# Optimization experiments

Hardware: AMD Instinct MI355X
Metric: run time of the kernel (lower is better)

Reference implementation:

```python
import jax, jax.numpy as jnp
import numpy as np

EPS = 2.220446049250313e-16  # sys.float_info.epsilon, matches CoCosNet feature_normalize

def feature_normalize(x):
    return x / (jnp.linalg.norm(x, axis=1, keepdims=True) + EPS)

def conv1x1(x, w, b):  # w: (out, in)
    return jnp.einsum('bchw,oc->bohw', x, w) + b[None, :, None, None]

def conv3x3(x, w, b):  # w: (out, in, 3, 3), SAME padding, stride 1
    y = jax.lax.conv_general_dilated(x, w, (1, 1), 'SAME',
                                     dimension_numbers=('NCHW', 'OIHW', 'NCHW'))
    return y + b[None, :, None, None]

@jax.custom_vjp
def sign_sig(x):
    return (x > 0).astype(x.dtype)

def _ss_fwd(x):
    return (x > 0).astype(x.dtype), jax.nn.sigmoid(x)

def _ss_bwd(s, g):
    return (g * s * (1.0 - s),)

sign_sig.defvjp(_ss_fwd, _ss_bwd)

def pono(x, eps=1e-5):  # PositionalNorm2d: normalize over channel dim
    m = jnp.mean(x, axis=1, keepdims=True)
    v = jnp.var(x, axis=1, keepdims=True)
    return (x - m) * jax.lax.rsqrt(v + eps)

def instance_norm(x, eps=1e-5):  # param-free, over spatial dims
    m = jnp.mean(x, axis=(2, 3), keepdims=True)
    v = jnp.var(x, axis=(2, 3), keepdims=True)
    return (x - m) * jax.lax.rsqrt(v + eps)

def setup_inputs() -> dict:
    B, CV, CPOS, H, W = 2, 256, 64, 64, 64
    CQK, DP, IC, NH = CV + CPOS, 64, 3, 128
    key = jax.random.key(0)
    ks = jax.random.split(key, 24)
    n = lambda i, s: jax.random.normal(ks[i], s, jnp.float32)
    w = lambda i, s: n(i, s) * 0.02
    z = lambda s: jnp.zeros(s, jnp.float32)
    return dict(
        q=n(0, (B, CV, H, W)), k=n(1, (B, CV, H, W)), v=n(2, (B, CV, H, W)),
        pos=n(3, (1, CPOS, H, W)),
        seg_map=jax.random.uniform(ks[4], (B, IC, H, W), jnp.float32),
        v2=n(5, (B, CV, H, W)),
        f_w=w(6, (CQK, CQK)), f_b=z(CQK),
        g_w=w(7, (CQK, CQK)), g_b=z(CQK),
        h_w=w(8, (CV, CV)), h_b=z(CV),
        fp_w=w(9, (DP, CQK)), fp_b=z(DP),
        gp_w=w(10, (DP, CQK)), gp_b=z(DP),
        sp_s_w=w(11, (NH, IC, 3, 3)), sp_s_b=z(NH),
        sp_g_w=w(12, (CV, NH, 3, 3)), sp_g_b=z(CV),
        sp_b_w=w(13, (CV, NH, 3, 3)), sp_b_b=z(CV),
        r1_w=w(14, (CV, CV, 3, 3)), r1_b=z(CV),
        r2_w=w(15, (CV, CV, 3, 3)), r2_b=z(CV),
    )

def reference(q, k, v, pos, seg_map, v2,
              f_w, f_b, g_w, g_b, h_w, h_b, fp_w, fp_b, gp_w, gp_b,
              sp_s_w, sp_s_b, sp_g_w, sp_g_b, sp_b_w, sp_b_b,
              r1_w, r1_b, r2_w, r2_b):
    b, cv, h, w = q.shape
    posb = jnp.broadcast_to(pos, (b,) + pos.shape[1:])
    query = jnp.concatenate([feature_normalize(q), posb], axis=1)
    keyt = jnp.concatenate([feature_normalize(k), posb], axis=1)
    qf = conv1x1(query, f_w, f_b)
    kf = conv1x1(keyt, g_w, g_b)
    vh = conv1x1(v, h_w, h_b)
    qp = conv1x1(query, fp_w, fp_b)
    kp = conv1x1(keyt, gp_w, gp_b)
    cqk = qf.shape[1]
    n = h * w
    Q = qf.reshape(b, cqk, n).transpose(0, 2, 1)          # (b, N, c_qk)
    K = kf.reshape(b, cqk, n)                             # (b, c_qk, N)
    V = vh.reshape(b, cv, n).transpose(0, 2, 1)           # (b, N, c_v)
    Qp = qp.reshape(b, -1, n).transpose(0, 2, 1)
    Kp = kp.reshape(b, -1, n)
    mask = sign_sig(jnp.einsum('bnc,bcm->bnm', Qp, Kp) / Kp.shape[1])
    cor = jnp.einsum('bnc,bcm->bnm', Q, K) / jnp.sqrt(jnp.float32(cqk))
    attn = jax.nn.softmax(cor, axis=-1)
    masked = attn * mask
    out = jnp.einsum('bnm,bmc->bnc', masked, V).transpose(0, 2, 1).reshape(b, cv, h, w)
    conf = masked.sum(-1).reshape(b, 1, h, w)
    V2 = v2.reshape(b, -1, n).transpose(0, 2, 1)
    attn2 = jax.nn.softmax(jnp.where(mask > 0, jnp.float32(-10000.0), cor), axis=-1)
    out2 = jnp.einsum('bnm,bmc->bnc', attn2, V2).transpose(0, 2, 1).reshape(b, -1, h, w)
    # SPADE(q, seg_map)
    actv = jax.nn.relu(conv3x3(seg_map, sp_s_w, sp_s_b))
    spade = instance_norm(q) * (1.0 + conv3x3(actv, sp_g_w, sp_g_b)) + conv3x3(actv, sp_b_w, sp_b_b)
    y = pono(out + (1.0 - conf) * spade + q)
    res = y + conv3x3(jax.nn.relu(conv3x3(y, r1_w, r1_b)), r2_w, r2_b)
    return (res, out2, cor)
```

## Files before the change

kernel.cpp:

```cpp
#include <hip/hip_runtime.h>
#include <stdint.h>


#define DEV static __device__ __forceinline__

typedef short short8 __attribute__((ext_vector_type(8)));
typedef float floatx4 __attribute__((ext_vector_type(4)));

DEV float bf2f(unsigned short b) { return __uint_as_float(((unsigned int)b) << 16); }
DEV unsigned short f2bf(float f) {
  unsigned int u = __float_as_uint(f);
  u += 0x7FFFu + ((u >> 16) & 1u);
  return (unsigned short)(u >> 16);
}
DEV float bfround(float f) { return bf2f(f2bf(f)); }

__global__ __launch_bounds__(256)
void cvt_f2b(const float* __restrict__ in, unsigned short* __restrict__ out, int n)
{
  int i = blockIdx.x * 256 + threadIdx.x;
  if (i < n) out[i] = f2bf(in[i]);
}

__global__ __launch_bounds__(256)
void prep_w9(const float* __restrict__ w, unsigned short* __restrict__ w9,
             int CO, int CI)
{
  int i = blockIdx.x * 256 + threadIdx.x;
  int tot = CO * CI * 9;
  if (i >= tot) return;
  int s = i % 9, rest = i / 9;
  int ci = rest % CI, o = rest / CI;
  w9[(long long)o * 9 * CI + s * CI + ci] = f2bf(w[i]);
}

__global__ __launch_bounds__(256)
void build_qk(const float* __restrict__ x, const float* __restrict__ pos,
              unsigned short* __restrict__ qt)
{
  int n = blockIdx.x, b = blockIdx.y, t = threadIdx.x;
  float v = x[((long long)(b * 256 + t) << 12) + n];
  __shared__ float red[256];
  red[t] = v * v; __syncthreads();
  for (int s = 128; s > 0; s >>= 1) { if (t < s) red[t] += red[t + s]; __syncthreads(); }
  float norm = sqrtf(red[0]) + 2.2204460492503131e-16f;
  unsigned short* orow = qt + ((long long)(b * 4096 + n)) * 320;
  orow[t] = f2bf(v / norm);
  if (t < 64) orow[256 + t] = f2bf(pos[t * 4096 + n]);
}

__global__ __launch_bounds__(256)
void transpose_c(const float* __restrict__ in, unsigned short* __restrict__ out, int C)
{
  __shared__ float tile[64][65];
  int b = blockIdx.z;
  int c0 = blockIdx.y << 6;
  int n0 = blockIdx.x << 6;
  const float* ib = in + (long long)b * C * 4096;
  unsigned short* ob = out + (long long)b * C * 4096;
  int tx = threadIdx.x & 63, tg = threadIdx.x >> 6;
#pragma unroll
  for (int i = 0; i < 16; i++) {
    int r = tg * 16 + i;
    tile[r][tx] = ib[((long long)(c0 + r) << 12) + n0 + tx];
  }
  __syncthreads();
#pragma unroll
  for (int i = 0; i < 16; i++) {
    int r = tg * 16 + i;
    ob[(long long)(n0 + r) * C + c0 + tx] = f2bf(tile[tx][r]);
  }
}

__global__ __launch_bounds__(256)
void gemm_bt(const unsigned short* __restrict__ A, long long sAb, int lda,
             const unsigned short* __restrict__ Bt, long long sBb, int ldb,
             int Ncols, int K, float alpha,
             const float* __restrict__ bias, int biasMode,
             unsigned short* __restrict__ Cb, long long sCbb, int ldcb,
             float* __restrict__ Cf, long long sCfb, int ldcf,
             unsigned short* __restrict__ Cm)
{
  __shared__ unsigned short As[128][40];
  __shared__ unsigned short Bs[128][40];
  int bz = blockIdx.z;
  const unsigned short* Ab = A + bz * sAb;
  const unsigned short* Bb = Bt + bz * sBb;
  int m0 = blockIdx.y << 7, n0 = blockIdx.x << 7;
  int t = threadIdx.x;
  int lane = t & 63, wave = t >> 6, quad = lane >> 4, l16 = lane & 15;
  int wm = (wave >> 1) << 6, wn = (wave & 1) << 6;

  floatx4 acc[4][4] = {};

  for (int k0 = 0; k0 < K; k0 += 32) {
#pragma unroll
    for (int s = 0; s < 2; s++) {
      int idx = t + (s << 8);
      int row = idx >> 2, ch = (idx & 3) << 3;
      short8 av = *(const short8*)(Ab + (long long)(m0 + row) * lda + k0 + ch);
      *(short8*)&As[row][ch] = av;
      short8 bv = {};
      if (n0 + row < Ncols) bv = *(const short8*)(Bb + (long long)(n0 + row) * ldb + k0 + ch);
      *(short8*)&Bs[row][ch] = bv;
    }
    __syncthreads();
    short8 af[4], bfv[4];
#pragma unroll
    for (int i = 0; i < 4; i++) af[i] = *(const short8*)&As[wm + (i << 4) + l16][quad << 3];
#pragma unroll
    for (int j = 0; j < 4; j++) bfv[j] = *(const short8*)&Bs[wn + (j << 4) + l16][quad << 3];
#pragma unroll
    for (int i = 0; i < 4; i++)
#pragma unroll
      for (int j = 0; j < 4; j++)
        acc[i][j] = __builtin_amdgcn_mfma_f32_16x16x32_bf16(af[i], bfv[j], acc[i][j], 0, 0, 0);
    __syncthreads();
  }

#pragma unroll
  for (int j = 0; j < 4; j++) {
    int col = n0 + wn + (j << 4) + l16;
    if (col >= Ncols) continue;
    float bcol = (biasMode == 1) ? bias[col] : 0.f;
#pragma unroll
    for (int i = 0; i < 4; i++) {
#pragma unroll
      for (int r = 0; r < 4; r++) {
        int row = m0 + wm + (i << 4) + (quad << 2) + r;
        float vv = acc[i][j][r] * alpha + bcol;
        if (biasMode == 2) vv += bias[row];
        if (Cb) Cb[bz * sCbb + (long long)row * ldcb + col] = f2bf(vv);
        if (Cf) Cf[bz * sCfb + (long long)row * ldcf + col] = bfround(vv);
        if (Cm) {
          unsigned long long bal = __ballot(vv > 0.f);
          if (l16 == 0)
            Cm[(long long)bz * 4096 * 256 + (long long)row * 256 + ((n0 + wn + (j << 4)) >> 4)]
              = (unsigned short)(bal >> (quad << 4));
        }
      }
    }
  }
}

__global__ __launch_bounds__(256)
void gemm_conv(const unsigned short* __restrict__ Xt, int CI,
               const unsigned short* __restrict__ W9, int CO,
               const float* __restrict__ bias,
               unsigned short* __restrict__ Cb, int relu,
               float* __restrict__ Cf, const float* __restrict__ addT, int rnd)
{
  __shared__ unsigned short As[128][40];
  __shared__ unsigned short Bs[128][40];
  int bz = blockIdx.z;
  const unsigned short* Xb = Xt + (long long)bz * 4096 * CI;
  int m0 = blockIdx.y << 7, n0 = blockIdx.x << 7;
  int t = threadIdx.x;
  int lane = t & 63, wave = t >> 6, quad = lane >> 4, l16 = lane & 15;
  int wm = (wave >> 1) << 6, wn = (wave & 1) << 6;
  int K9 = 9 * CI;

  floatx4 acc[4][4] = {};

  for (int tap = 0; tap < 9; ++tap) {
    int dy = tap / 3 - 1, dx = tap % 3 - 1;
    int off = dy * 64 + dx;
    for (int kc = 0; kc < CI; kc += 32) {
#pragma unroll
      for (int s = 0; s < 2; s++) {
        int idx = t + (s << 8);
        int row = idx >> 2, ch = (idx & 3) << 3;
        int p = m0 + row;
        int y = (p >> 6) + dy, x = (p & 63) + dx;
        short8 av = {};
        if ((unsigned)y < 64u && (unsigned)x < 64u)
          av = *(const short8*)(Xb + (long long)(p + off) * CI + kc + ch);
        *(short8*)&As[row][ch] = av;
        short8 bv = *(const short8*)(W9 + (long long)(n0 + row) * K9 + tap * CI + kc + ch);
        *(short8*)&Bs[row][ch] = bv;
      }
      __syncthreads();
      short8 af[4], bfv[4];
#pragma unroll
      for (int i = 0; i < 4; i++) af[i] = *(const short8*)&As[wm + (i << 4) + l16][quad << 3];
#pragma unroll
      for (int j = 0; j < 4; j++) bfv[j] = *(const short8*)&Bs[wn + (j << 4) + l16][quad << 3];
#pragma unroll
      for (int i = 0; i < 4; i++)
#pragma unroll
        for (int j = 0; j < 4; j++)
          acc[i][j] = __builtin_amdgcn_mfma_f32_16x16x32_bf16(af[i], bfv[j], acc[i][j], 0, 0, 0);
      __syncthreads();
    }
  }

#pragma unroll
  for (int j = 0; j < 4; j++) {
    int col = n0 + wn + (j << 4) + l16;
    float bcol = bias[col];
#pragma unroll
    for (int i = 0; i < 4; i++) {
#pragma unroll
      for (int r = 0; r < 4; r++) {
        int row = m0 + wm + (i << 4) + (quad << 2) + r;
        float vv = acc[i][j][r] + bcol;
        if (relu) vv = fmaxf(vv, 0.f);
        if (Cb) Cb[((long long)bz * 4096 + row) * CO + col] = f2bf(vv);
        if (Cf) {
          long long oi = ((long long)bz * CO + col) * 4096 + row;
          float ov = vv;
          if (addT) ov += addT[oi];
          Cf[oi] = rnd ? bfround(ov) : ov;
        }
      }
    }
  }
}

__global__ __launch_bounds__(256)
void stats_rows(const float* __restrict__ corF,
                const unsigned char* __restrict__ mbits,
                float4* __restrict__ statA, float* __restrict__ confF)
{
  long long row = blockIdx.x;
  const float4* cr = (const float4*)(corF + (row << 12));
  const unsigned char* mr = mbits + row * 512;
  int t = threadIdx.x;

  float lg[16]; unsigned int mk[16];
#pragma unroll
  for (int i = 0; i < 4; i++) {
    float4 cc = cr[i * 256 + t];
    unsigned char mb = mr[(i * 256 + t) >> 1];
    int sh = (t & 1) << 2;
    lg[4 * i + 0] = cc.x; lg[4 * i + 1] = cc.y;
    lg[4 * i + 2] = cc.z; lg[4 * i + 3] = cc.w;
#pragma unroll
    for (int j = 0; j < 4; j++) mk[4 * i + j] = (mb >> (sh + j)) & 1u;
  }
  float m1 = -3.0e38f, m2 = -3.0e38f; int cnt = 0;
#pragma unroll
  for (int e = 0; e < 16; e++) {
    m1 = fmaxf(m1, lg[e]);
    if (!mk[e]) m2 = fmaxf(m2, lg[e]);
    cnt += (int)mk[e];
  }
  __shared__ float4 red4[256];
  red4[t] = make_float4(m1, m2, 0.f, 0.f); __syncthreads();
  for (int s = 128; s > 0; s >>= 1) {
    if (t < s) {
      red4[t].x = fmaxf(red4[t].x, red4[t + s].x);
      red4[t].y = fmaxf(red4[t].y, red4[t + s].y);
    }
    __syncthreads();
  }
  float rmax1 = red4[0].x;
  float rmax2 = fmaxf(red4[0].y, -10000.f);
  __syncthreads();

  float s1 = 0.f, cn = 0.f, s2 = 0.f;
#pragma unroll
  for (int e = 0; e < 16; e++) {
    float ex = __expf(fminf(lg[e] - rmax1, 0.f));
    s1 += ex;
    if (mk[e]) cn += ex;
    else s2 += __expf(fminf(lg[e] - rmax2, 0.f));
  }
  red4[t] = make_float4(s1, cn, s2, (float)cnt); __syncthreads();
  for (int s = 128; s > 0; s >>= 1) {
    if (t < s) {
      red4[t].x += red4[t + s].x; red4[t].y += red4[t + s].y;
      red4[t].z += red4[t + s].z; red4[t].w += red4[t + s].w;
    }
    __syncthreads();
  }
  if (t == 0) {
    float4 r = red4[0];
    float sum2 = r.z + r.w * __expf(fminf(-10000.f - rmax2, 0.f));
    statA[row] = make_float4(rmax1, 1.f / fmaxf(r.x, 1e-30f),
                             rmax2, 1.f / fmaxf(sum2, 1e-30f));
    confF[row] = r.y / fmaxf(r.x, 1e-30f);
  }
}

__global__ __launch_bounds__(256)
void gemm_pv2(const float* __restrict__ corF,
              const unsigned char* __restrict__ mbits,
              const float4* __restrict__ statA,
              const unsigned short* __restrict__ Bt0,
              const unsigned short* __restrict__ Bt1,
              float* __restrict__ Cf0, float* __restrict__ Cf1)
{
  __shared__ unsigned short As[64][40];
  __shared__ unsigned short Bs[128][40];
  int bz = blockIdx.z & 1, mode = blockIdx.z >> 1;
  const float* corb = corF + (long long)bz * 4096 * 4096;
  const unsigned char* mbb = mbits + (long long)bz * 4096 * 512;
  const unsigned short* Bb = (mode ? Bt1 : Bt0) + (long long)bz * 256 * 4096;
  int m0 = blockIdx.y << 6, n0 = blockIdx.x << 7;
  int t = threadIdx.x;
  int lane = t & 63, wave = t >> 6, quad = lane >> 4, l16 = lane & 15;
  int wm = (wave >> 1) << 5, wn = (wave & 1) << 6;

  int rA = t >> 2, cA = (t & 3) << 3;

  float4 sS = statA[(long long)bz * 4096 + m0 + rA];
  float rm, iv, mv;
  if (mode == 0) { rm = sS.x; iv = sS.y; mv = 0.f; }
  else { rm = sS.z; iv = sS.w; mv = __expf(fminf(-10000.f - rm, 0.f)) * iv; }

  floatx4 acc[2][4] = {};

  float4 pa0, pa1; short8 pb0, pb1; unsigned char pmb;
  auto issue = [&](int kk) {
    const float* cp = corb + (long long)(m0 + rA) * 4096 + kk + cA;
    pa0 = *(const float4*)cp;
    pa1 = *(const float4*)(cp + 4);
    pmb = mbb[(long long)(m0 + rA) * 512 + ((kk + cA) >> 3)];
    pb0 = *(const short8*)(Bb + (long long)(n0 + rA) * 4096 + kk + cA);
    pb1 = *(const short8*)(Bb + (long long)(n0 + rA + 64) * 4096 + kk + cA);
  };

  issue(0);
  for (int k0 = 0; k0 < 4096; k0 += 32) {
    {
      float cs[8] = {pa0.x, pa0.y, pa0.z, pa0.w, pa1.x, pa1.y, pa1.z, pa1.w};
      short8 av;
#pragma unroll
      for (int j = 0; j < 8; j++) {
        float p = __expf(fminf(cs[j] - rm, 0.f)) * iv;
        unsigned int mkb = (pmb >> j) & 1u;
        float val = mode ? (mkb ? mv : p) : (mkb ? p : 0.f);
        av[j] = (short)f2bf(val);
      }
      *(short8*)&As[rA][cA] = av;
      *(short8*)&Bs[rA][cA] = pb0;
      *(short8*)&Bs[rA + 64][cA] = pb1;
    }
    __syncthreads();
    if (k0 + 32 < 4096) issue(k0 + 32);
    short8 af[2], bfv[4];
#pragma unroll
    for (int i = 0; i < 2; i++) af[i] = *(const short8*)&As[wm + (i << 4) + l16][quad << 3];
#pragma unroll
    for (int j = 0; j < 4; j++) bfv[j] = *(const short8*)&Bs[wn + (j << 4) + l16][quad << 3];
#pragma unroll
    for (int i = 0; i < 2; i++)
#pragma unroll
      for (int j = 0; j < 4; j++)
        acc[i][j] = __builtin_amdgcn_mfma_f32_16x16x32_bf16(af[i], bfv[j], acc[i][j], 0, 0, 0);
    __syncthreads();
  }

#pragma unroll
  for (int j = 0; j < 4; j++) {
    int col = n0 + wn + (j << 4) + l16;
#pragma unroll
    for (int i = 0; i < 2; i++) {
#pragma unroll
      for (int r = 0; r < 4; r++) {
        int row = m0 + wm + (i << 4) + (quad << 2) + r;
        float vv = bfround(acc[i][j][r]);
        if (mode) Cf1[(long long)bz * 256 * 4096 + (long long)col * 4096 + row] = vv;
        else      Cf0[(long long)bz * 4096 * 256 + (long long)row * 256 + col] = vv;
      }
    }
  }
}

__global__ __launch_bounds__(256)
void inorm_stats(const float* __restrict__ q, float* __restrict__ mu, float* __restrict__ rs)
{
  int c = blockIdx.x, b = blockIdx.y, t = threadIdx.x;
  const float* base = q + ((long long)(b * 256 + c) << 12);
  float s = 0.f, s2 = 0.f;
  for (int i = t; i < 4096; i += 256) { float v = base[i]; s += v; s2 += v * v; }
  __shared__ float r1[256], r2[256];
  r1[t] = s; r2[t] = s2; __syncthreads();
  for (int st = 128; st > 0; st >>= 1) {
    if (t < st) { r1[t] += r1[t + st]; r2[t] += r2[t + st]; }
    __syncthreads();
  }
  if (t == 0) {
    float m = r1[0] * (1.f / 4096.f);
    float var = fmaxf(r2[0] * (1.f / 4096.f) - m * m, 0.f);
    mu[b * 256 + c] = m;
    rs[b * 256 + c] = rsqrtf(var + 1e-5f);
  }
}

__global__ __launch_bounds__(256)
void conv3x3(const float* __restrict__ inF,
             const float* __restrict__ wgt, const float* __restrict__ bias,
             int CI, int CO, const float* __restrict__ addF,
             float* __restrict__ outF, int relu, int rnd)
{
  __shared__ float wsm[2304];
  int b = blockIdx.z, o = blockIdx.y, t = threadIdx.x;
  for (int i = t; i < CI * 9; i += 256) wsm[i] = wgt[(long long)o * CI * 9 + i];
  __syncthreads();
  int x = t & 63, y = (blockIdx.x << 2) + (t >> 6);
  bool ym = y > 0, yp = y < 63, xm = x > 0, xp = x < 63;
  int p = y * 64 + x;
  long long ibase = ((long long)b * CI) << 12;
  float acc = bias[o];
  for (int ci = 0; ci < CI; ci++) {
    const float* wp = &wsm[ci * 9];
    long long ib = ibase + ((long long)ci << 12) + p;
    float v00 = (ym && xm) ? inF[ib - 65] : 0.f;
    float v01 = ym ? inF[ib - 64] : 0.f;
    float v02 = (ym && xp) ? inF[ib - 63] : 0.f;
    float v10 = xm ? inF[ib - 1] : 0.f;
    float v11 = inF[ib];
    float v12 = xp ? inF[ib + 1] : 0.f;
    float v20 = (yp && xm) ? inF[ib + 63] : 0.f;
    float v21 = yp ? inF[ib + 64] : 0.f;
    float v22 = (yp && xp) ? inF[ib + 65] : 0.f;
    acc += v00 * wp[0] + v01 * wp[1] + v02 * wp[2]
         + v10 * wp[3] + v11 * wp[4] + v12 * wp[5]
         + v20 * wp[6] + v21 * wp[7] + v22 * wp[8];
  }
  if (relu) acc = fmaxf(acc, 0.f);
  long long oidx = (((long long)(b * CO + o)) << 12) + p;
  if (addF) acc += addF[oidx];
  outF[oidx] = rnd ? bfround(acc) : acc;
}

__global__ __launch_bounds__(256)
void pono_y(const float* __restrict__ outF, const float* __restrict__ confF,
            const float* __restrict__ gF, const float* __restrict__ bF,
            const float* __restrict__ q, const float* __restrict__ mu,
            const float* __restrict__ rs, float* __restrict__ yF,
            unsigned short* __restrict__ yT)
{
  int n = blockIdx.x, b = blockIdx.y, c = threadIdx.x;
  long long cn = ((long long)(b * 256 + c) << 12) + n;
  float qv = q[cn];
  float sp = (qv - mu[b * 256 + c]) * rs[b * 256 + c] * (1.f + gF[cn]) + bF[cn];
  float cf = confF[b * 4096 + n];
  float tv = outF[((long long)(b * 4096 + n) << 8) + c] + (1.f - cf) * sp + qv;
  __shared__ float red[256];
  red[c] = tv; __syncthreads();
  for (int s = 128; s > 0; s >>= 1) { if (c < s) red[c] += red[c + s]; __syncthreads(); }
  float m = red[0] * (1.f / 256.f); __syncthreads();
  float d = tv - m;
  red[c] = d * d; __syncthreads();
  for (int s = 128; s > 0; s >>= 1) { if (c < s) red[c] += red[c + s]; __syncthreads(); }
  float var = fmaxf(red[0] * (1.f / 256.f), 0.f);
  float yv = d * rsqrtf(var + 1e-5f);
  yF[cn] = yv;
  yT[((long long)(b * 4096 + n) << 8) + c] = f2bf(yv);
}


extern "C" void kernel_launch(void* const* d_in, const int* in_sizes, int n_in,
                              void* d_out, int out_size, void* d_ws, size_t ws_size,
                              hipStream_t stream)
{
  (void)in_sizes; (void)n_in; (void)out_size; (void)ws_size;
  const int B = 2, CV = 256, CQK = 320, DP = 64, N = 4096, NH = 128, IC = 3;
  const float INV_SQRT_CQK = 0.05590169943749474241f;

  const float* q    = (const float*)d_in[0];
  const float* k    = (const float*)d_in[1];
  const float* v    = (const float*)d_in[2];
  const float* pos  = (const float*)d_in[3];
  const float* seg  = (const float*)d_in[4];
  const float* v2   = (const float*)d_in[5];
  const float* f_w  = (const float*)d_in[6];
  const float* f_b  = (const float*)d_in[7];
  const float* g_w  = (const float*)d_in[8];
  const float* g_b  = (const float*)d_in[9];
  const float* h_w  = (const float*)d_in[10];
  const float* h_b  = (const float*)d_in[11];
  const float* fp_w = (const float*)d_in[12];
  const float* fp_b = (const float*)d_in[13];
  const float* gp_w = (const float*)d_in[14];
  const float* gp_b = (const float*)d_in[15];
  const float* sp_s_w = (const float*)d_in[16];
  const float* sp_s_b = (const float*)d_in[17];
  const float* sp_g_w = (const float*)d_in[18];
  const float* sp_g_b = (const float*)d_in[19];
  const float* sp_b_w = (const float*)d_in[20];
  const float* sp_b_b = (const float*)d_in[21];
  const float* r1_w = (const float*)d_in[22];
  const float* r1_b = (const float*)d_in[23];
  const float* r2_w = (const float*)d_in[24];
  const float* r2_b = (const float*)d_in[25];

  float* res_o  = (float*)d_out;
  float* out2_o = res_o + (long long)B * CV * N;
  float* cor_o  = res_o + 2ll * B * CV * N;

  unsigned short* query_t = (unsigned short*)cor_o;
  unsigned short* keyt_t  = query_t + (long long)B * N * CQK;
  float*          outBuf  = res_o;

  char* wp_ = (char*)d_ws;
  auto take = [&](size_t bytes) -> void* {
    void* r = wp_; wp_ += (bytes + 255) & ~(size_t)255; return r;
  };
  unsigned short* v_t     = (unsigned short*)take((size_t)B * N * CV * 2);
  unsigned short* qf_t    = (unsigned short*)take((size_t)B * N * CQK * 2);
  unsigned short* kf_t    = (unsigned short*)take((size_t)B * N * CQK * 2);
  unsigned short* qp_t    = (unsigned short*)take((size_t)B * N * DP * 2);
  unsigned short* kp_t    = (unsigned short*)take((size_t)B * N * DP * 2);
  unsigned short* vh      = (unsigned short*)take((size_t)B * CV * N * 2);
  unsigned short* v2b     = (unsigned short*)take((size_t)B * CV * N * 2);
  unsigned short* fwB     = (unsigned short*)take((size_t)CQK * CQK * 2);
  unsigned short* gwB     = (unsigned short*)take((size_t)CQK * CQK * 2);
  unsigned short* fpwB    = (unsigned short*)take((size_t)DP * CQK * 2);
  unsigned short* gpwB    = (unsigned short*)take((size_t)DP * CQK * 2);
  unsigned short* hwB     = (unsigned short*)take((size_t)CV * CV * 2);
  unsigned short* maskB16 = (unsigned short*)take((size_t)B * N * 256 * 2);
  float4*         statA   = (float4*)take((size_t)B * N * 16);
  float*          confF   = (float*)take((size_t)B * N * 4);
  float*          muF     = (float*)take((size_t)B * CV * 4);
  float*          rsF     = (float*)take((size_t)B * CV * 4);
  float*          actv    = (float*)take((size_t)B * NH * N * 4);
  float*          gC      = (float*)take((size_t)B * CV * N * 4);
  float*          bC      = (float*)take((size_t)B * CV * N * 4);
  float*          yF      = (float*)take((size_t)B * CV * N * 4);
  unsigned short* spgW9   = (unsigned short*)take((size_t)CV * 9 * NH * 2);
  unsigned short* spbW9   = (unsigned short*)take((size_t)CV * 9 * NH * 2);
  unsigned short* r1W9    = (unsigned short*)take((size_t)CV * 9 * CV * 2);
  unsigned short* r2W9    = (unsigned short*)take((size_t)CV * 9 * CV * 2);
  unsigned short* yT      = qf_t;
  unsigned short* a1T     = kf_t;
  unsigned short* actvT   = v_t;

  dim3 blk(256);
  auto cvt = [&](const float* in, unsigned short* out, int n) {
    cvt_f2b<<<dim3((n + 255) / 256), blk, 0, stream>>>(in, out, n);
  };
  auto prepw = [&](const float* w, unsigned short* w9, int CO, int CI) {
    prep_w9<<<dim3((CO * CI * 9 + 255) / 256), blk, 0, stream>>>(w, w9, CO, CI);
  };
  auto gemm = [&](const unsigned short* A, long long sAb, int lda,
                  const unsigned short* Bt, long long sBb, int ldb,
                  int M, int Nc, int K, float alpha,
                  const float* bias, int biasMode,
                  unsigned short* Cb, long long sCbb, int ldcb,
                  float* Cf, long long sCfb, int ldcf,
                  unsigned short* Cm) {
    dim3 grid((Nc + 127) / 128, M / 128, B);
    gemm_bt<<<grid, blk, 0, stream>>>(A, sAb, lda, Bt, sBb, ldb, Nc, K, alpha,
                                      bias, biasMode, Cb, sCbb, ldcb,
                                      Cf, sCfb, ldcf, Cm);
  };
  auto conv = [&](const unsigned short* Xt, int CI, const unsigned short* W9,
                  const float* bias, unsigned short* Cb, int relu,
                  float* Cf, const float* addT, int rnd) {
    gemm_conv<<<dim3(CV / 128, N / 128, B), blk, 0, stream>>>(
        Xt, CI, W9, CV, bias, Cb, relu, Cf, addT, rnd);
  };

  cvt(f_w, fwB, CQK * CQK);
  cvt(g_w, gwB, CQK * CQK);
  cvt(fp_w, fpwB, DP * CQK);
  cvt(gp_w, gpwB, DP * CQK);
  cvt(h_w, hwB, CV * CV);
  cvt(v2, v2b, B * CV * N);
  prepw(sp_g_w, spgW9, CV, NH);
  prepw(sp_b_w, spbW9, CV, NH);
  prepw(r1_w, r1W9, CV, CV);
  prepw(r2_w, r2W9, CV, CV);

  build_qk<<<dim3(N, B), blk, 0, stream>>>(q, pos, query_t);
  build_qk<<<dim3(N, B), blk, 0, stream>>>(k, pos, keyt_t);
  transpose_c<<<dim3(64, 4, B), blk, 0, stream>>>(v, v_t, CV);

  gemm(query_t, (long long)N * CQK, CQK, fwB, 0, CQK, N, CQK, CQK, 1.f, f_b, 1,
       qf_t, (long long)N * CQK, CQK, nullptr, 0, 0, nullptr);
  gemm(keyt_t, (long long)N * CQK, CQK, gwB, 0, CQK, N, CQK, CQK, 1.f, g_b, 1,
       kf_t, (long long)N * CQK, CQK, nullptr, 0, 0, nullptr);
  gemm(query_t, (long long)N * CQK, CQK, fpwB, 0, CQK, N, DP, CQK, 1.f, fp_b, 1,
       qp_t, (long long)N * DP, DP, nullptr, 0, 0, nullptr);
  gemm(keyt_t, (long long)N * CQK, CQK, gpwB, 0, CQK, N, DP, CQK, 1.f, gp_b, 1,
       kp_t, (long long)N * DP, DP, nullptr, 0, 0, nullptr);
  gemm(hwB, 0, CV, v_t, (long long)N * CV, CV, CV, N, CV, 1.f, h_b, 2,
       vh, (long long)CV * N, N, nullptr, 0, 0, nullptr);

  gemm(qf_t, (long long)N * CQK, CQK, kf_t, (long long)N * CQK, CQK, N, N, CQK,
       INV_SQRT_CQK, nullptr, 0, nullptr, 0, 0,
       cor_o, (long long)N * N, N, nullptr);
  gemm(qp_t, (long long)N * DP, DP, kp_t, (long long)N * DP, DP, N, N, DP, 1.f,
       nullptr, 0, nullptr, 0, 0, nullptr, 0, 0, maskB16);

  stats_rows<<<dim3(B * N), blk, 0, stream>>>(cor_o, (const unsigned char*)maskB16,
                                              statA, confF);
  gemm_pv2<<<dim3(2, 64, 2 * B), blk, 0, stream>>>(
      cor_o, (const unsigned char*)maskB16, statA, vh, v2b, outBuf, out2_o);

  inorm_stats<<<dim3(CV, B), blk, 0, stream>>>(q, muF, rsF);
  conv3x3<<<dim3(16, NH, B), blk, 0, stream>>>(seg, sp_s_w, sp_s_b, IC, NH, nullptr, actv, 1, 0);
  transpose_c<<<dim3(64, 2, B), blk, 0, stream>>>(actv, actvT, NH);
  conv(actvT, NH, spgW9, sp_g_b, nullptr, 0, gC, nullptr, 0);
  conv(actvT, NH, spbW9, sp_b_b, nullptr, 0, bC, nullptr, 0);
  pono_y<<<dim3(N, B), blk, 0, stream>>>(outBuf, confF, gC, bC, q, muF, rsF, yF, yT);
  conv(yT, CV, r1W9, r1_b, a1T, 1, nullptr, nullptr, 0);
  conv(a1T, CV, r2W9, r2_b, nullptr, 0, res_o, yF, 1);
}
```

Before: 844.8 us.

## Split qk normalization into coalesced colnorm plus tiled transpose; retile PV GEMM

The per-pixel build_qk kernel, which read channels with a 16KB stride, is replaced by two kernels. colnorm computes per-pixel inverse norms with coalesced reads, and build_qk3 transposes 64x64 tiles through shared memory, applying the scale and appending pos. The PV GEMM now uses 128-thread blocks with a 32-row M tile and a launch_bounds occupancy hint, which doubles the grid for more parallelism. It also drops the fminf clamp inside exp; the row max should make that clamp redundant, but each block now reloads the same B tile for half as many rows.

```diff
diff --git a/kernel.cpp b/kernel.cpp
--- a/kernel.cpp
+++ b/kernel.cpp
@@ -35,18 +35,52 @@
 }
 
 __global__ __launch_bounds__(256)
-void build_qk(const float* __restrict__ x, const float* __restrict__ pos,
-              unsigned short* __restrict__ qt)
-{
-  int n = blockIdx.x, b = blockIdx.y, t = threadIdx.x;
-  float v = x[((long long)(b * 256 + t) << 12) + n];
+void colnorm(const float* __restrict__ x, float* __restrict__ rnorm)
+{
+  int b = blockIdx.y, t = threadIdx.x;
+  int n = (blockIdx.x << 5) + (t & 31);
+  int cg = t >> 5;
+  const float* base = x + ((long long)b << 20) + n;
+  float s = 0.f;
+#pragma unroll
+  for (int c8 = 0; c8 < 32; c8++) {
+    float v = base[((long long)(cg * 32 + c8)) << 12];
+    s += v * v;
+  }
   __shared__ float red[256];
-  red[t] = v * v; __syncthreads();
-  for (int s = 128; s > 0; s >>= 1) { if (t < s) red[t] += red[t + s]; __syncthreads(); }
-  float norm = sqrtf(red[0]) + 2.2204460492503131e-16f;
-  unsigned short* orow = qt + ((long long)(b * 4096 + n)) * 320;
-  orow[t] = f2bf(v / norm);
-  if (t < 64) orow[256 + t] = f2bf(pos[t * 4096 + n]);
+  red[t] = s; __syncthreads();
+  for (int st = 128; st >= 32; st >>= 1) {
+    if (t < st) red[t] += red[t + st];
+    __syncthreads();
+  }
+  if (t < 32)
+    rnorm[(b << 12) + n] = 1.f / (sqrtf(red[t]) + 2.2204460492503131e-16f);
+}
+
+__global__ __launch_bounds__(256)
+void build_qk3(const float* __restrict__ x, const float* __restrict__ pos,
+               const float* __restrict__ rnorm, unsigned short* __restrict__ qt)
+{
+  __shared__ float tile[64][65];
+  int b = blockIdx.z, by = blockIdx.y;
+  int n0 = blockIdx.x << 6;
+  int tx = threadIdx.x & 63, tg = threadIdx.x >> 6;
+  const float* ib;
+  int c0;
+  if (by < 4) { ib = x + ((long long)b << 20) + ((long long)(by << 6) << 12); c0 = by << 6; }
+  else        { ib = pos; c0 = 256; }
+#pragma unroll
+  for (int i = 0; i < 16; i++) {
+    int r = tg * 16 + i;
+    tile[r][tx] = ib[((long long)r << 12) + n0 + tx];
+  }
+  __syncthreads();
+#pragma unroll
+  for (int i = 0; i < 16; i++) {
+    int r = tg * 16 + i;
+    float sc = (by < 4) ? rnorm[(b << 12) + n0 + r] : 1.f;
+    qt[((long long)(b * 4096 + n0 + r)) * 320 + c0 + tx] = f2bf(tile[tx][r] * sc);
+  }
 }
 
 __global__ __launch_bounds__(256)
@@ -283,24 +317,24 @@
   }
 }
 
-__global__ __launch_bounds__(256)
-void gemm_pv2(const float* __restrict__ corF,
+__global__ __launch_bounds__(128, 3)
+void gemm_pv3(const float* __restrict__ corF,
               const unsigned char* __restrict__ mbits,
               const float4* __restrict__ statA,
               const unsigned short* __restrict__ Bt0,
               const unsigned short* __restrict__ Bt1,
               float* __restrict__ Cf0, float* __restrict__ Cf1)
 {
-  __shared__ unsigned short As[64][40];
+  __shared__ unsigned short As[32][40];
   __shared__ unsigned short Bs[128][40];
   int bz = blockIdx.z & 1, mode = blockIdx.z >> 1;
   const float* corb = corF + (long long)bz * 4096 * 4096;
   const unsigned char* mbb = mbits + (long long)bz * 4096 * 512;
   const unsigned short* Bb = (mode ? Bt1 : Bt0) + (long long)bz * 256 * 4096;
-  int m0 = blockIdx.y << 6, n0 = blockIdx.x << 7;
+  int m0 = blockIdx.y << 5, n0 = blockIdx.x << 7;
   int t = threadIdx.x;
   int lane = t & 63, wave = t >> 6, quad = lane >> 4, l16 = lane & 15;
-  int wm = (wave >> 1) << 5, wn = (wave & 1) << 6;
+  int wn = wave << 6;
 
   int rA = t >> 2, cA = (t & 3) << 3;
 
@@ -311,14 +345,18 @@
 
   floatx4 acc[2][4] = {};
 
-  float4 pa0, pa1; short8 pb0, pb1; unsigned char pmb;
+  const float* cp_base = corb + (long long)(m0 + rA) * 4096 + cA;
+  const unsigned char* mb_base = mbb + (long long)(m0 + rA) * 512 + (cA >> 3);
+  const unsigned short* pb_base = Bb + (long long)(n0 + rA) * 4096 + cA;
+
+  float4 pa0, pa1; short8 pb[4]; unsigned char pmb;
   auto issue = [&](int kk) {
-    const float* cp = corb + (long long)(m0 + rA) * 4096 + kk + cA;
-    pa0 = *(const float4*)cp;
-    pa1 = *(const float4*)(cp + 4);
-    pmb = mbb[(long long)(m0 + rA) * 512 + ((kk + cA) >> 3)];
-    pb0 = *(const short8*)(Bb + (long long)(n0 + rA) * 4096 + kk + cA);
-    pb1 = *(const short8*)(Bb + (long long)(n0 + rA + 64) * 4096 + kk + cA);
+    pa0 = *(const float4*)(cp_base + kk);
+    pa1 = *(const float4*)(cp_base + kk + 4);
+    pmb = mb_base[kk >> 3];
+#pragma unroll
+    for (int j = 0; j < 4; j++)
+      pb[j] = *(const short8*)(pb_base + (long long)(j << 5) * 4096 + kk);
   };
 
   issue(0);
@@ -328,20 +366,21 @@
       short8 av;
 #pragma unroll
       for (int j = 0; j < 8; j++) {
-        float p = __expf(fminf(cs[j] - rm, 0.f)) * iv;
+        float p = __expf(cs[j] - rm) * iv;
         unsigned int mkb = (pmb >> j) & 1u;
         float val = mode ? (mkb ? mv : p) : (mkb ? p : 0.f);
         av[j] = (short)f2bf(val);
       }
       *(short8*)&As[rA][cA] = av;
-      *(short8*)&Bs[rA][cA] = pb0;
-      *(short8*)&Bs[rA + 64][cA] = pb1;
+#pragma unroll
+      for (int j = 0; j < 4; j++)
+        *(short8*)&Bs[rA + (j << 5)][cA] = pb[j];
     }
     __syncthreads();
     if (k0 + 32 < 4096) issue(k0 + 32);
     short8 af[2], bfv[4];
 #pragma unroll
-    for (int i = 0; i < 2; i++) af[i] = *(const short8*)&As[wm + (i << 4) + l16][quad << 3];
+    for (int i = 0; i < 2; i++) af[i] = *(const short8*)&As[(i << 4) + l16][quad << 3];
 #pragma unroll
     for (int j = 0; j < 4; j++) bfv[j] = *(const short8*)&Bs[wn + (j << 4) + l16][quad << 3];
 #pragma unroll
@@ -359,7 +398,7 @@
     for (int i = 0; i < 2; i++) {
 #pragma unroll
       for (int r = 0; r < 4; r++) {
-        int row = m0 + wm + (i << 4) + (quad << 2) + r;
+        int row = m0 + (i << 4) + (quad << 2) + r;
         float vv = bfround(acc[i][j][r]);
         if (mode) Cf1[(long long)bz * 256 * 4096 + (long long)col * 4096 + row] = vv;
         else      Cf0[(long long)bz * 4096 * 256 + (long long)row * 256 + col] = vv;
@@ -517,6 +556,8 @@
   float*          confF   = (float*)take((size_t)B * N * 4);
   float*          muF     = (float*)take((size_t)B * CV * 4);
   float*          rsF     = (float*)take((size_t)B * CV * 4);
+  float*          rnormQ  = (float*)take((size_t)B * N * 4);
+  float*          rnormK  = (float*)take((size_t)B * N * 4);
   float*          actv    = (float*)take((size_t)B * NH * N * 4);
   float*          gC      = (float*)take((size_t)B * CV * N * 4);
   float*          bC      = (float*)take((size_t)B * CV * N * 4);
@@ -566,8 +607,10 @@
   prepw(r1_w, r1W9, CV, CV);
   prepw(r2_w, r2W9, CV, CV);
 
-  build_qk<<<dim3(N, B), blk, 0, stream>>>(q, pos, query_t);
-  build_qk<<<dim3(N, B), blk, 0, stream>>>(k, pos, keyt_t);
+  colnorm<<<dim3(128, B), blk, 0, stream>>>(q, rnormQ);
+  colnorm<<<dim3(128, B), blk, 0, stream>>>(k, rnormK);
+  build_qk3<<<dim3(64, 5, B), blk, 0, stream>>>(q, pos, rnormQ, query_t);
+  build_qk3<<<dim3(64, 5, B), blk, 0, stream>>>(k, pos, rnormK, keyt_t);
   transpose_c<<<dim3(64, 4, B), blk, 0, stream>>>(v, v_t, CV);
 
   gemm(query_t, (long long)N * CQK, CQK, fwB, 0, CQK, N, CQK, CQK, 1.f, f_b, 1,
@@ -589,7 +632,7 @@
 
   stats_rows<<<dim3(B * N), blk, 0, stream>>>(cor_o, (const unsigned char*)maskB16,
                                               statA, confF);
-  gemm_pv2<<<dim3(2, 64, 2 * B), blk, 0, stream>>>(
+  gemm_pv3<<<dim3(2, 128, 2 * B), dim3(128), 0, stream>>>(
       cor_o, (const unsigned char*)maskB16, statA, vh, v2b, outBuf, out2_o);
 
   inorm_stats<<<dim3(CV, B), blk, 0, stream>>>(q, muF, rsF);
```

Result: no change. 838.7 us (-0.7%).
